# Optimization experiments

Hardware: AMD Instinct MI355X
Metric: run time of the kernel (lower is better)

Reference implementation:

```python
import jax, jax.numpy as jnp
import numpy as np

H = 8  # num_attention_heads
DH = 64  # attention_head_size
D = H * DH  # hidden_size = 512
LN_EPS = 1e-6


def setup_inputs() -> dict:
    key = jax.random.key(0)
    ks = jax.random.split(key, 12)
    B, L = 32, 196
    s = 1.0 / np.sqrt(D)
    return {
        "query_states": jax.random.normal(ks[0], (B, L, D), jnp.float32),
        "key_states": jax.random.normal(ks[1], (B, L, D), jnp.float32),
        "value_states": jax.random.normal(ks[2], (B, L, D), jnp.float32),
        "Wq": jax.random.normal(ks[3], (D, D), jnp.float32) * s,
        "bq": jnp.zeros((D,), jnp.float32),
        "Wk": jax.random.normal(ks[4], (D, D), jnp.float32) * s,
        "bk": jnp.zeros((D,), jnp.float32),
        "Wv": jax.random.normal(ks[5], (D, D), jnp.float32) * s,
        "bv": jnp.zeros((D,), jnp.float32),
        "ln_gamma": jnp.ones((D,), jnp.float32),
        "ln_beta": jnp.zeros((D,), jnp.float32),
        "logit_scale": jnp.ones((), jnp.float32),
    }


def _heads(x):
    # (B, L, D) -> (B, H, L, DH)
    B, L, _ = x.shape
    return x.reshape(B, L, H, DH).transpose(0, 2, 1, 3)


def reference(query_states, key_states, value_states, Wq, bq, Wk, bk, Wv, bv,
              ln_gamma, ln_beta, logit_scale):
    B, L, _ = query_states.shape
    q = _heads(query_states @ Wq.T + bq)  # (B,H,L,DH)
    k = _heads(key_states @ Wk.T + bk)
    v = _heads(value_states @ Wv.T + bv)

    # cross-batch retrieval: sum over heads and head_dim -> (a,b,l,m)
    retrieve = jnp.einsum('ahld,bhmd->ablm', q, k)
    mask_sum = jnp.float32(L)  # mask is all-ones (B, L)
    t2v = retrieve.max(axis=-1).sum(axis=2) / mask_sum  # (a,b)
    v2t = retrieve.max(axis=-2).sum(axis=2) / mask_sum  # (a,b)
    retrieve_logits = jnp.exp(logit_scale) * (t2v + v2t) / 2.0

    # self-attention (dropout is identity in eval)
    scores = jnp.einsum('bhld,bhmd->bhlm', q, k) / jnp.sqrt(jnp.float32(DH))
    probs = jax.nn.softmax(scores, axis=-1)  # (B,H,L,L)
    ctx = jnp.einsum('bhlm,bhmd->bhld', probs, v)
    ctx = ctx.transpose(0, 2, 1, 3).reshape(B, L, D)
    ctx = ctx + query_states

    mu = ctx.mean(axis=-1, keepdims=True)
    var = ((ctx - mu) ** 2).mean(axis=-1, keepdims=True)
    ctx = (ctx - mu) / jnp.sqrt(var + LN_EPS) * ln_gamma + ln_beta

    return ctx, retrieve_logits, probs.mean(axis=1)
```

## Files before the change

kernel.cpp:

```cpp
#include <hip/hip_runtime.h>
#include <hip/hip_bf16.h>

#define BB 32
#define LL 196
#define DD 512
#define HH 8
#define DHH 64
#define BL (BB*LL)
#define PVK 224
#define PSTR 236
#define CSTR 528

typedef __bf16 bf16x8 __attribute__((ext_vector_type(8)));
typedef float f32x4 __attribute__((ext_vector_type(4)));

#define MFMA16(a,b,c) __builtin_amdgcn_mfma_f32_16x16x32_bf16((a),(b),(c),0,0,0)

#define GLOAD_LDS16(g, l) __builtin_amdgcn_global_load_lds( \
    (const __attribute__((address_space(1))) void*)(g), \
    (__attribute__((address_space(3))) void*)(l), 16, 0, 0)

static __device__ __forceinline__ bf16x8 pack8(float4 v0, float4 v1) {
  bf16x8 o;
  o[0] = (__bf16)v0.x; o[1] = (__bf16)v0.y; o[2] = (__bf16)v0.z; o[3] = (__bf16)v0.w;
  o[4] = (__bf16)v1.x; o[5] = (__bf16)v1.y; o[6] = (__bf16)v1.z; o[7] = (__bf16)v1.w;
  return o;
}

static __device__ __forceinline__ unsigned fkey(float f) {
  unsigned u = __float_as_uint(f);
  return u ^ ((unsigned)((int)u >> 31) | 0x80000000u);
}
static __device__ __forceinline__ float unkey(unsigned k) {
  unsigned u = (k & 0x80000000u) ? (k ^ 0x80000000u) : ~k;
  return __uint_as_float(u);
}

#define STAGE_PAIR(SA, SB, abase, bbase) do { \
  const __bf16* aB_ = (abase); const __bf16* bB_ = (bbase); \
  _Pragma("unroll") \
  for (int c_ = 0; c_ < 4; ++c_) { \
    const int p_ = c_ * 256 + tid; \
    GLOAD_LDS16(aB_ + (size_t)(p_ >> 3) * DD + swoff, &SA[p_ * 8]); \
  } \
  _Pragma("unroll") \
  for (int c_ = 0; c_ < 4; ++c_) { \
    const int p_ = c_ * 256 + tid; \
    GLOAD_LDS16(bB_ + (size_t)(p_ >> 3) * DD + swoff, &SB[p_ * 8]); \
  } \
} while (0)

#define COMPUTE_TILE(SA, SB) do { \
  _Pragma("unroll") \
  for (int kc_ = 0; kc_ < 2; ++kc_) { \
    const int q_ = (((kc_ * 4 + (lane >> 4)) ^ (lane & 7)) << 3); \
    bf16x8 af_[4], bf_[4]; \
    _Pragma("unroll") \
    for (int mt_ = 0; mt_ < 4; ++mt_) \
      af_[mt_] = *(const bf16x8*)&SA[(wr + mt_ * 16 + (lane & 15)) * 64 + q_]; \
    _Pragma("unroll") \
    for (int nt_ = 0; nt_ < 4; ++nt_) \
      bf_[nt_] = *(const bf16x8*)&SB[(wc + nt_ * 16 + (lane & 15)) * 64 + q_]; \
    _Pragma("unroll") \
    for (int mt_ = 0; mt_ < 4; ++mt_) \
      _Pragma("unroll") \
      for (int nt_ = 0; nt_ < 4; ++nt_) \
        acc[mt_][nt_] = MFMA16(af_[mt_], bf_[nt_], acc[mt_][nt_]); \
  } \
} while (0)

__global__ __launch_bounds__(256) void cvt_kernel(
    const float* __restrict__ x0, const float* __restrict__ x1, const float* __restrict__ x2,
    const float* __restrict__ w0, const float* __restrict__ w1, const float* __restrict__ w2,
    __bf16* __restrict__ xb, __bf16* __restrict__ wb)
{
  const int z = blockIdx.y;
  const float* src; __bf16* dst; size_t i;
  if (blockIdx.x < 1568) {
    src = (z == 0) ? x0 : (z == 1) ? x1 : x2;
    dst = xb + (size_t)z * 3211264;
    i = (size_t)blockIdx.x * 256 + threadIdx.x;
  } else {
    src = (z == 0) ? w0 : (z == 1) ? w1 : w2;
    dst = wb + (size_t)z * 262144;
    i = (size_t)(blockIdx.x - 1568) * 256 + threadIdx.x;
  }
  const float4* s = (const float4*)(src + i * 8);
  float4 a = s[0], b = s[1];
  *(bf16x8*)(dst + i * 8) = pack8(a, b);
}

__global__ __launch_bounds__(256) void proj_gemm_kernel(
    const __bf16* __restrict__ xb, const __bf16* __restrict__ wb,
    const float* __restrict__ bq, const float* __restrict__ bk, const float* __restrict__ bv,
    __bf16* __restrict__ qp, __bf16* __restrict__ kp, __bf16* __restrict__ vp)
{
  __shared__ __bf16 sA[128 * 64];
  __shared__ __bf16 sB[128 * 64];

  const int z = blockIdx.z;
  const __bf16* A = xb + (size_t)z * 3211264;
  const __bf16* B = wb + (size_t)z * 262144;
  const float* bias = (z == 0) ? bq : (z == 1) ? bk : bv;
  __bf16* out = (z == 0) ? qp : (z == 1) ? kp : vp;

  const int tid = threadIdx.x;
  const int w = tid >> 6, lane = tid & 63;
  const int wr = (w >> 1) * 64, wc = (w & 1) * 64;
  const int bm = blockIdx.x * 128, bn = blockIdx.y * 128;
  const int swoff = ((tid & 7) ^ ((tid >> 3) & 7)) << 3;

  const __bf16* aP = A + (size_t)bm * DD;
  const __bf16* bP = B + (size_t)bn * DD;

  f32x4 acc[4][4] = {};

  #pragma unroll
  for (int kt = 0; kt < 8; ++kt) {
    STAGE_PAIR(sA, sB, aP + kt * 64, bP + kt * 64);
    __syncthreads();
    COMPUTE_TILE(sA, sB);
    __syncthreads();
  }

  #pragma unroll
  for (int mt = 0; mt < 4; ++mt)
    #pragma unroll
    for (int nt = 0; nt < 4; ++nt)
      #pragma unroll
      for (int rr = 0; rr < 4; ++rr) {
        const int row = bm + wr + mt * 16 + (lane >> 4) * 4 + rr;
        const int col = bn + wc + nt * 16 + (lane & 15);
        out[(size_t)row * DD + col] = (__bf16)(acc[mt][nt][rr] + bias[col]);
      }
}

__global__ __launch_bounds__(256) void transpose_v_kernel(
    const __bf16* __restrict__ vp, __bf16* __restrict__ vpT)
{
  __shared__ __bf16 sT[64][72];
  const int bbh = blockIdx.x;
  const int mt = blockIdx.y;
  const int bb = bbh >> 3, h = bbh & 7;
  const int tid = threadIdx.x;
  {
    const int r = tid >> 2, c0 = (tid & 3) * 16;
    const int m = mt * 64 + r;
    bf16x8 z = {};
    bf16x8 v0 = z, v1 = z;
    if (m < LL) {
      const bf16x8* src = (const bf16x8*)&vp[(size_t)(bb * LL + m) * DD + h * DHH + c0];
      v0 = src[0]; v1 = src[1];
    }
    *(bf16x8*)&sT[r][c0]     = v0;
    *(bf16x8*)&sT[r][c0 + 8] = v1;
  }
  __syncthreads();
  {
    const int d = tid >> 2, mc0 = (tid & 3) * 16;
    if (mt * 64 + mc0 < PVK) {
      bf16x8 o0, o1;
      #pragma unroll
      for (int j = 0; j < 8; ++j) { o0[j] = sT[mc0 + j][d]; o1[j] = sT[mc0 + 8 + j][d]; }
      __bf16* dst = vpT + (size_t)(bbh * 64 + d) * PVK + mt * 64 + mc0;
      *(bf16x8*)dst = o0;
      *(bf16x8*)(dst + 8) = o1;
    }
  }
}

__global__ __launch_bounds__(256) void retrieve_kernel(
    const __bf16* __restrict__ qp, const __bf16* __restrict__ kp,
    unsigned* __restrict__ rmax, unsigned* __restrict__ cmax)
{
  __shared__ __bf16 sA[128 * 64];
  __shared__ __bf16 sB[128 * 64];

  const int orig = blockIdx.x;
  const int xcd = orig & 7, idx = orig >> 3;
  const int wg = (xcd == 0) ? idx : (301 + (xcd - 1) * 300 + idx);
  const int st = wg / 49, wi = wg % 49;
  const int brow = ((st / 7) * 7 + wi / 7) * 128;
  const int bcol = ((st % 7) * 7 + wi % 7) * 128;

  const int tid = threadIdx.x;
  const int w = tid >> 6, lane = tid & 63;
  const int wr = (w >> 1) * 64, wc = (w & 1) * 64;
  const int swoff = ((tid & 7) ^ ((tid >> 3) & 7)) << 3;

  const __bf16* aP = qp + (size_t)brow * DD;
  const __bf16* bP = kp + (size_t)bcol * DD;

  f32x4 acc[4][4] = {};

  #pragma unroll
  for (int kt = 0; kt < 8; ++kt) {
    STAGE_PAIR(sA, sB, aP + kt * 64, bP + kt * 64);
    __syncthreads();
    COMPUTE_TILE(sA, sB);
    __syncthreads();
  }

  const int wcol0 = bcol + wc;
  const int wrow0 = brow + wr;
  {
    const int b0 = wcol0 / LL, b1 = (wcol0 + 63) / LL;
    for (int b = b0; b <= b1; ++b) {
      const int lo = b * LL, hi = lo + LL;
      #pragma unroll
      for (int mt = 0; mt < 4; ++mt)
        #pragma unroll
        for (int rr = 0; rr < 4; ++rr) {
          float m = -3e38f;
          #pragma unroll
          for (int nt = 0; nt < 4; ++nt) {
            const int col = wcol0 + nt * 16 + (lane & 15);
            if (col >= lo && col < hi) m = fmaxf(m, acc[mt][nt][rr]);
          }
          m = fmaxf(m, __shfl_xor(m, 1));
          m = fmaxf(m, __shfl_xor(m, 2));
          m = fmaxf(m, __shfl_xor(m, 4));
          m = fmaxf(m, __shfl_xor(m, 8));
          if ((lane & 15) == 0) {
            const int grow = wrow0 + mt * 16 + (lane >> 4) * 4 + rr;
            atomicMax(&rmax[(size_t)b * BL + grow], fkey(m));
          }
        }
    }
  }
  {
    const int a0 = wrow0 / LL, a1 = (wrow0 + 63) / LL;
    for (int a = a0; a <= a1; ++a) {
      const int lo = a * LL, hi = lo + LL;
      #pragma unroll
      for (int nt = 0; nt < 4; ++nt) {
        float cm = -3e38f;
        #pragma unroll
        for (int mt = 0; mt < 4; ++mt)
          #pragma unroll
          for (int rr = 0; rr < 4; ++rr) {
            const int grow = wrow0 + mt * 16 + (lane >> 4) * 4 + rr;
            if (grow >= lo && grow < hi) cm = fmaxf(cm, acc[mt][nt][rr]);
          }
        cm = fmaxf(cm, __shfl_xor(cm, 16));
        cm = fmaxf(cm, __shfl_xor(cm, 32));
        if (lane < 16) {
          const int col = wcol0 + nt * 16 + lane;
          atomicMax(&cmax[(size_t)a * BL + col], fkey(cm));
        }
      }
    }
  }
}

__global__ __launch_bounds__(256) void finish_kernel(
    const unsigned* __restrict__ rmax, const unsigned* __restrict__ cmax,
    const float* __restrict__ ls, float* __restrict__ out_logits)
{
  const int tid = threadIdx.x;
  const int w = tid >> 6, lane = tid & 63;
  const int pair = blockIdx.x * 4 + w;
  const int a = pair >> 5, b = pair & 31;
  float s = 0.f;
  #pragma unroll
  for (int k = 0; k < 4; ++k) {
    const int l = lane + k * 64;
    if (l < LL) {
      s += unkey(rmax[(size_t)b * BL + a * LL + l]);
      s += unkey(cmax[(size_t)a * BL + b * LL + l]);
    }
  }
  #pragma unroll
  for (int o = 1; o < 64; o <<= 1) s += __shfl_xor(s, o);
  if (lane == 0)
    out_logits[a * BB + b] = expf(ls[0]) * s * (0.5f / (float)LL);
}

__global__ __launch_bounds__(512) void attn_kernel(
    const __bf16* __restrict__ qp, const __bf16* __restrict__ kp,
    const __bf16* __restrict__ vpT, const float* __restrict__ resid,
    const float* __restrict__ gamma, const float* __restrict__ beta,
    float* __restrict__ out_ctx, float* __restrict__ probs_out)
{
  __shared__ __align__(16) char smem[8 * 16 * PSTR * 2];
  auto pr    = (__bf16(*)[16][PSTR])smem;
  auto ctile = (float(*)[CSTR])smem;

  const int bb = blockIdx.x;
  const int strip = blockIdx.y;
  const int tid = threadIdx.x;
  const int w = tid >> 6, lane = tid & 63;
  const int h = w;
  const int row0 = strip * 16;

  for (int i = lane; i < 256; i += 64)
    pr[w][i >> 4][208 + (i & 15)] = (__bf16)0.f;

  const int arow = row0 + (lane & 15);
  const bool aval = arow < LL;

  bf16x8 aq[2];
  #pragma unroll
  for (int kc = 0; kc < 2; ++kc) {
    bf16x8 z = {};
    aq[kc] = aval
      ? *(const bf16x8*)&qp[(size_t)(bb * LL + arow) * DD + h * DHH + kc * 32 + (lane >> 4) * 8]
      : z;
  }
  f32x4 s[13] = {};
  __builtin_amdgcn_s_setprio(1);
  #pragma unroll
  for (int nt = 0; nt < 13; ++nt) {
    const int brow = nt * 16 + (lane & 15);
    #pragma unroll
    for (int kc = 0; kc < 2; ++kc) {
      bf16x8 bk = {};
      if (brow < LL)
        bk = *(const bf16x8*)&kp[(size_t)(bb * LL + brow) * DD + h * DHH + kc * 32 + (lane >> 4) * 8];
      s[nt] = MFMA16(aq[kc], bk, s[nt]);
    }
  }
  __builtin_amdgcn_s_setprio(0);

  const int colbase = lane & 15;
  #pragma unroll
  for (int nt = 0; nt < 13; ++nt) {
    const bool cv = (nt * 16 + colbase) < LL;
    #pragma unroll
    for (int rr = 0; rr < 4; ++rr)
      s[nt][rr] = cv ? s[nt][rr] * 0.125f : -1e30f;
  }
  float mx[4], dn[4];
  #pragma unroll
  for (int rr = 0; rr < 4; ++rr) {
    float m = s[0][rr];
    #pragma unroll
    for (int nt = 1; nt < 13; ++nt) m = fmaxf(m, s[nt][rr]);
    m = fmaxf(m, __shfl_xor(m, 1));
    m = fmaxf(m, __shfl_xor(m, 2));
    m = fmaxf(m, __shfl_xor(m, 4));
    m = fmaxf(m, __shfl_xor(m, 8));
    mx[rr] = m;
  }
  #pragma unroll
  for (int nt = 0; nt < 13; ++nt)
    #pragma unroll
    for (int rr = 0; rr < 4; ++rr)
      s[nt][rr] = __expf(s[nt][rr] - mx[rr]);
  #pragma unroll
  for (int rr = 0; rr < 4; ++rr) {
    float d = 0.f;
    #pragma unroll
    for (int nt = 0; nt < 13; ++nt) d += s[nt][rr];
    d += __shfl_xor(d, 1);
    d += __shfl_xor(d, 2);
    d += __shfl_xor(d, 4);
    d += __shfl_xor(d, 8);
    dn[rr] = 1.f / d;
  }
  #pragma unroll
  for (int nt = 0; nt < 13; ++nt)
    #pragma unroll
    for (int rr = 0; rr < 4; ++rr)
      pr[w][(lane >> 4) * 4 + rr][nt * 16 + colbase] = (__bf16)(s[nt][rr] * dn[rr]);
  __syncthreads();

  f32x4 c4[4] = {};
  __builtin_amdgcn_s_setprio(1);
  #pragma unroll
  for (int kc = 0; kc < 7; ++kc) {
    bf16x8 ap = *(const bf16x8*)&pr[w][lane & 15][kc * 32 + (lane >> 4) * 8];
    #pragma unroll
    for (int dt = 0; dt < 4; ++dt) {
      bf16x8 bv = *(const bf16x8*)&vpT[(size_t)((bb * 8 + h) * 64 + dt * 16 + (lane & 15)) * PVK + kc * 32 + (lane >> 4) * 8];
      c4[dt] = MFMA16(ap, bv, c4[dt]);
    }
  }
  __builtin_amdgcn_s_setprio(0);

  {
    const int rr_ = tid >> 5;
    const int qrow = row0 + rr_;
    if (qrow < LL) {
      #pragma unroll
      for (int j = 0; j < 7; ++j) {
        const int c = (tid & 31) + j * 32;
        if (c < LL) {
          float sum = 0.f;
          #pragma unroll
          for (int ww = 0; ww < 8; ++ww) sum += (float)pr[ww][rr_][c];
          probs_out[((size_t)bb * LL + qrow) * LL + c] = sum * 0.125f;
        }
      }
    }
  }
  __syncthreads();

  #pragma unroll
  for (int dt = 0; dt < 4; ++dt)
    #pragma unroll
    for (int rr = 0; rr < 4; ++rr)
      ctile[(lane >> 4) * 4 + rr][h * DHH + dt * 16 + (lane & 15)] = c4[dt][rr];
  __syncthreads();

  #pragma unroll
  for (int rsel = 0; rsel < 2; ++rsel) {
    const int r = w * 2 + rsel;
    const int qrow = row0 + r;
    if (qrow >= LL) continue;
    const int c = lane * 8;
    const float* rrow = resid + (size_t)(bb * LL + qrow) * DD;
    float4 a0 = *(const float4*)&ctile[r][c];
    float4 a1 = *(const float4*)&ctile[r][c + 4];
    float4 b0 = *(const float4*)(rrow + c);
    float4 b1 = *(const float4*)(rrow + c + 4);
    float v[8] = {a0.x + b0.x, a0.y + b0.y, a0.z + b0.z, a0.w + b0.w,
                  a1.x + b1.x, a1.y + b1.y, a1.z + b1.z, a1.w + b1.w};
    float sum = 0.f;
    #pragma unroll
    for (int j = 0; j < 8; ++j) sum += v[j];
    #pragma unroll
    for (int o = 1; o < 64; o <<= 1) sum += __shfl_xor(sum, o);
    const float mu = sum * (1.f / (float)DD);
    float var = 0.f;
    #pragma unroll
    for (int j = 0; j < 8; ++j) { float d = v[j] - mu; var += d * d; }
    #pragma unroll
    for (int o = 1; o < 64; o <<= 1) var += __shfl_xor(var, o);
    const float rstd = rsqrtf(var * (1.f / (float)DD) + 1e-6f);
    float4 g0 = *(const float4*)(gamma + c);
    float4 g1 = *(const float4*)(gamma + c + 4);
    float4 e0 = *(const float4*)(beta + c);
    float4 e1 = *(const float4*)(beta + c + 4);
    float g[8] = {g0.x, g0.y, g0.z, g0.w, g1.x, g1.y, g1.z, g1.w};
    float e[8] = {e0.x, e0.y, e0.z, e0.w, e1.x, e1.y, e1.z, e1.w};
    float o_[8];
    #pragma unroll
    for (int j = 0; j < 8; ++j) o_[j] = (v[j] - mu) * rstd * g[j] + e[j];
    float* orow = out_ctx + (size_t)(bb * LL + qrow) * DD;
    *(float4*)(orow + c)     = make_float4(o_[0], o_[1], o_[2], o_[3]);
    *(float4*)(orow + c + 4) = make_float4(o_[4], o_[5], o_[6], o_[7]);
  }
}

extern "C" void kernel_launch(void* const* d_in, const int* in_sizes, int n_in,
                              void* d_out, int out_size, void* d_ws, size_t ws_size,
                              hipStream_t stream)
{
  const float* xq    = (const float*)d_in[0];
  const float* xk    = (const float*)d_in[1];
  const float* xv    = (const float*)d_in[2];
  const float* Wq    = (const float*)d_in[3];
  const float* bq    = (const float*)d_in[4];
  const float* Wk    = (const float*)d_in[5];
  const float* bk    = (const float*)d_in[6];
  const float* Wv    = (const float*)d_in[7];
  const float* bv    = (const float*)d_in[8];
  const float* gamma = (const float*)d_in[9];
  const float* beta  = (const float*)d_in[10];
  const float* ls    = (const float*)d_in[11];

  float* out_ctx    = (float*)d_out;
  float* out_logits = out_ctx + (size_t)BL * DD;
  float* out_probs  = out_logits + BB * BB;

  const size_t xsz = (size_t)BL * DD;
  const size_t wsz = (size_t)DD * DD;
  __bf16* xb = (__bf16*)d_ws;
  __bf16* wb = xb + 3 * xsz;
  __bf16* qp = wb + 3 * wsz;
  __bf16* kp = qp + xsz;
  __bf16* vp = kp + xsz;
  __bf16* vpT = xb;
  unsigned* rmax = (unsigned*)(xb + 3670016);
  unsigned* cmax = rmax + (size_t)BB * BL;

  cvt_kernel<<<dim3(1696, 3), 256, 0, stream>>>(xq, xk, xv, Wq, Wk, Wv, xb, wb);

  proj_gemm_kernel<<<dim3(49, 4, 3), 256, 0, stream>>>(xb, wb, bq, bk, bv, qp, kp, vp);

  transpose_v_kernel<<<dim3(BB * HH, 4), 256, 0, stream>>>(vp, vpT);

  hipMemsetAsync(rmax, 0, (size_t)2 * BB * BL * sizeof(unsigned), stream);

  retrieve_kernel<<<2401, 256, 0, stream>>>(qp, kp, rmax, cmax);
  finish_kernel<<<256, 256, 0, stream>>>(rmax, cmax, ls, out_logits);

  attn_kernel<<<dim3(BB, 13), 512, 0, stream>>>(qp, kp, vpT, xq, gamma, beta,
                                                out_ctx, out_probs);
}
```

Baseline: 232.2 us.

## Fuse logits finish into attention kernel, prefetch V fragments, vectorize probs mean

Removes the separate finish kernel launch by computing the retrieval logits reduction at the tail of the attention kernel, using 4 waves in each of the first 8 strips per batch. It also preloads all V-transposed MFMA operands into registers at kernel start, so the global loads overlap the QK/softmax phase instead of stalling the PV loop. The head-averaged probs write now reads 8 bf16 values at a time and stores float4s. The register prefetch (28 bf16x8 per lane) raises register pressure in a 512-thread kernel and may force spills.

```diff
diff --git a/kernel.cpp b/kernel.cpp
--- a/kernel.cpp
+++ b/kernel.cpp
@@ -253,34 +253,14 @@
   }
 }
 
-__global__ __launch_bounds__(256) void finish_kernel(
-    const unsigned* __restrict__ rmax, const unsigned* __restrict__ cmax,
-    const float* __restrict__ ls, float* __restrict__ out_logits)
-{
-  const int tid = threadIdx.x;
-  const int w = tid >> 6, lane = tid & 63;
-  const int pair = blockIdx.x * 4 + w;
-  const int a = pair >> 5, b = pair & 31;
-  float s = 0.f;
-  #pragma unroll
-  for (int k = 0; k < 4; ++k) {
-    const int l = lane + k * 64;
-    if (l < LL) {
-      s += unkey(rmax[(size_t)b * BL + a * LL + l]);
-      s += unkey(cmax[(size_t)a * BL + b * LL + l]);
-    }
-  }
-  #pragma unroll
-  for (int o = 1; o < 64; o <<= 1) s += __shfl_xor(s, o);
-  if (lane == 0)
-    out_logits[a * BB + b] = expf(ls[0]) * s * (0.5f / (float)LL);
-}
-
 __global__ __launch_bounds__(512) void attn_kernel(
     const __bf16* __restrict__ qp, const __bf16* __restrict__ kp,
     const __bf16* __restrict__ vpT, const float* __restrict__ resid,
     const float* __restrict__ gamma, const float* __restrict__ beta,
-    float* __restrict__ out_ctx, float* __restrict__ probs_out)
+    const unsigned* __restrict__ rmax, const unsigned* __restrict__ cmax,
+    const float* __restrict__ ls,
+    float* __restrict__ out_ctx, float* __restrict__ probs_out,
+    float* __restrict__ out_logits)
 {
   __shared__ __align__(16) char smem[8 * 16 * PSTR * 2];
   auto pr    = (__bf16(*)[16][PSTR])smem;
@@ -293,6 +273,14 @@
   const int h = w;
   const int row0 = strip * 16;
 
+  bf16x8 bvf[4][7];
+  #pragma unroll
+  for (int dt = 0; dt < 4; ++dt)
+    #pragma unroll
+    for (int kc = 0; kc < 7; ++kc)
+      bvf[dt][kc] = *(const bf16x8*)&vpT[(size_t)((bb * 8 + h) * 64 + dt * 16 + (lane & 15)) * PVK
+                                          + kc * 32 + (lane >> 4) * 8];
+
   for (int i = lane; i < 256; i += 64)
     pr[w][i >> 4][208 + (i & 15)] = (__bf16)0.f;
 
@@ -371,25 +359,31 @@
   for (int kc = 0; kc < 7; ++kc) {
     bf16x8 ap = *(const bf16x8*)&pr[w][lane & 15][kc * 32 + (lane >> 4) * 8];
     #pragma unroll
-    for (int dt = 0; dt < 4; ++dt) {
-      bf16x8 bv = *(const bf16x8*)&vpT[(size_t)((bb * 8 + h) * 64 + dt * 16 + (lane & 15)) * PVK + kc * 32 + (lane >> 4) * 8];
-      c4[dt] = MFMA16(ap, bv, c4[dt]);
-    }
+    for (int dt = 0; dt < 4; ++dt)
+      c4[dt] = MFMA16(ap, bvf[dt][kc], c4[dt]);
   }
   __builtin_amdgcn_s_setprio(0);
 
   {
-    const int rr_ = tid >> 5;
-    const int qrow = row0 + rr_;
-    if (qrow < LL) {
-      #pragma unroll
-      for (int j = 0; j < 7; ++j) {
-        const int c = (tid & 31) + j * 32;
-        if (c < LL) {
-          float sum = 0.f;
+    if (tid < 448) {
+      const int row = tid / 28, ch = tid % 28, c0 = ch * 8;
+      const int qrow = row0 + row;
+      if (qrow < LL && c0 < LL) {
+        float sm[8] = {};
+        #pragma unroll
+        for (int ww = 0; ww < 8; ++ww) {
+          bf16x8 v = *(const bf16x8*)&pr[ww][row][c0];
           #pragma unroll
-          for (int ww = 0; ww < 8; ++ww) sum += (float)pr[ww][rr_][c];
-          probs_out[((size_t)bb * LL + qrow) * LL + c] = sum * 0.125f;
+          for (int j = 0; j < 8; ++j) sm[j] += (float)v[j];
+        }
+        float* dst = &probs_out[((size_t)bb * LL + qrow) * LL + c0];
+        if (c0 + 8 <= LL) {
+          *(float4*)dst       = make_float4(sm[0] * 0.125f, sm[1] * 0.125f, sm[2] * 0.125f, sm[3] * 0.125f);
+          *(float4*)(dst + 4) = make_float4(sm[4] * 0.125f, sm[5] * 0.125f, sm[6] * 0.125f, sm[7] * 0.125f);
+        } else {
+          #pragma unroll
+          for (int j = 0; j < 8; ++j)
+            if (c0 + j < LL) dst[j] = sm[j] * 0.125f;
         }
       }
     }
@@ -440,6 +434,23 @@
     float* orow = out_ctx + (size_t)(bb * LL + qrow) * DD;
     *(float4*)(orow + c)     = make_float4(o_[0], o_[1], o_[2], o_[3]);
     *(float4*)(orow + c + 4) = make_float4(o_[4], o_[5], o_[6], o_[7]);
+  }
+
+  if (strip < 8 && w < 4) {
+    const int a = bb, b = strip * 4 + w;
+    float s2 = 0.f;
+    #pragma unroll
+    for (int k = 0; k < 4; ++k) {
+      const int l = lane + k * 64;
+      if (l < LL) {
+        s2 += unkey(rmax[(size_t)b * BL + a * LL + l]);
+        s2 += unkey(cmax[(size_t)a * BL + b * LL + l]);
+      }
+    }
+    #pragma unroll
+    for (int o = 1; o < 64; o <<= 1) s2 += __shfl_xor(s2, o);
+    if (lane == 0)
+      out_logits[a * BB + b] = expf(ls[0]) * s2 * (0.5f / (float)LL);
   }
 }
 
@@ -484,8 +495,8 @@
   hipMemsetAsync(rmax, 0, (size_t)2 * BB * BL * sizeof(unsigned), stream);
 
   retrieve_kernel<<<2401, 256, 0, stream>>>(qp, kp, rmax, cmax);
-  finish_kernel<<<256, 256, 0, stream>>>(rmax, cmax, ls, out_logits);
 
   attn_kernel<<<dim3(BB, 13), 512, 0, stream>>>(qp, kp, vpT, xq, gamma, beta,
-                                                out_ctx, out_probs);
-}
+                                                rmax, cmax, ls,
+                                                out_ctx, out_probs, out_logits);
+}
```

Result: no change. 231.1 us (-0.5%).
